# Kernel tuning notes

Measured on AMD Instinct MI355X. Metric: run time of the kernel, lower is better.

## Reference

```python
import jax, jax.numpy as jnp
import numpy as np
from jax import lax

NOISE_STD = 0.0005
ALPHA = 0.1
B, S, I, H, O = 128, 2000, 8, 512, 2
NUM_EXC, NUM_INH = 384, 128


def setup_inputs() -> dict:
    key = jax.random.key(0)
    ks = jax.random.split(key, 6)
    return {
        "input": jax.random.normal(ks[0], (B, S, I), dtype=jnp.float32),
        "noise": jax.random.normal(ks[1], (B, S, H), dtype=jnp.float32),
        "wi": jax.random.normal(ks[2], (I, H), dtype=jnp.float32) / np.sqrt(I),
        # excitatory rows in [0, 0.5], inhibitory rows in [-0.5, 0] (Dale's law)
        "wrec_exc": jax.random.uniform(ks[3], (NUM_EXC, H), dtype=jnp.float32, minval=0.0, maxval=0.5),
        "wrec_inh": jax.random.uniform(ks[4], (NUM_INH, H), dtype=jnp.float32, minval=-0.5, maxval=0.0),
        "wout": jax.random.normal(ks[5], (H, O), dtype=jnp.float32) / np.sqrt(H),
        "h0": jnp.zeros((H,), dtype=jnp.float32),
    }


def reference(input, noise, wi, wrec_exc, wrec_inh, wout, h0):
    batch = input.shape[0]
    # wrec rows: [exc sources; inh sources]
    wrec = jnp.concatenate([wrec_exc, wrec_inh], axis=0)  # [H, H]
    r0 = jnp.tanh(h0)  # [H]
    out0 = jnp.broadcast_to(r0 @ wout, (batch, wout.shape[1]))  # output[:, 0]
    h_init = jnp.broadcast_to(h0, (batch, h0.shape[0]))  # [B, H]
    # precompute input projection for steps 0..S-2 (last step's input unused)
    xproj = jnp.einsum("bsi,ih->sbh", input[:, :-1], wi)  # [S-1, B, H]
    noise_t = jnp.transpose(noise[:, :-1], (1, 0, 2))  # [S-1, B, H]

    def step(h, inp):
        x_t, n_t = inp
        r = jnp.tanh(h)
        h_new = h + NOISE_STD * n_t + ALPHA * (-h + r @ wrec.T + x_t)
        return h_new, jnp.tanh(h_new) @ wout  # emit output[:, i+1]

    _, outs = lax.scan(step, h_init, (xproj, noise_t))  # outs: [S-1, B, O]
    output = jnp.concatenate([out0[None], outs], axis=0)  # [S, B, O]
    return jnp.transpose(output, (1, 0, 2))  # [B, S, O]
```

## Files before the change

### kernel.cpp

```cpp
#include <hip/hip_runtime.h>
#include <cmath>


constexpr int kS = 2000, kI = 8, kH = 512, kO = 2;
constexpr float kNoiseStd = 0.0005f, kAlpha = 0.1f;

constexpr int GROUPS = 8;
constexpr int NSPL   = 2;
constexpr int JS     = 256;
constexpr int NTHR   = 512;
constexpr int NBLK   = GROUPS * NSPL;
constexpr int RSLOT  = 8192;

typedef _Float16 half8  __attribute__((ext_vector_type(8)));
typedef float    floatx4 __attribute__((ext_vector_type(4)));
typedef unsigned uintx4  __attribute__((ext_vector_type(4)));

#define MFMA16(A, B, C) __builtin_amdgcn_mfma_f32_16x16x32_f16((A), (B), (C), 0, 0, 0)
#define PIN8(a) asm volatile("" : "+v"((a)[0]), "+v"((a)[1]), "+v"((a)[2]), "+v"((a)[3]), \
                                   "+v"((a)[4]), "+v"((a)[5]), "+v"((a)[6]), "+v"((a)[7]))

static __device__ __forceinline__ unsigned ld_flag(const unsigned* p) {
  return __hip_atomic_load(p, __ATOMIC_RELAXED, __HIP_MEMORY_SCOPE_AGENT);
}
static __device__ __forceinline__ void st_flag(unsigned* p, unsigned v) {
  __hip_atomic_store(p, v, __ATOMIC_RELAXED, __HIP_MEMORY_SCOPE_AGENT);
}

static __device__ __forceinline__ float fast_tanh(float x) {
  const float ax = __builtin_fabsf(x);
  const float e = __builtin_amdgcn_exp2f(2.8853900817779268f * ax);
  const float r = __builtin_amdgcn_rcpf(e + 1.0f);
  return __builtin_copysignf(__builtin_fmaf(-2.0f, r, 1.0f), x);
}

__global__ __launch_bounds__(NTHR, 1) void rnn_k(
    const float* __restrict__ inp,
    const float* __restrict__ noise,
    const float* __restrict__ wi,
    const float* __restrict__ wexc,
    const float* __restrict__ winh,
    const float* __restrict__ wout,
    const float* __restrict__ h0,
    float* __restrict__ out,
    _Float16* __restrict__ rbuf,
    unsigned* __restrict__ flags)
{
  const int bid = blockIdx.x;
  const int g = bid & 7;
  const int c = bid >> 3;
  const int tid = threadIdx.x;
  const int w = tid >> 6;
  const int lane = tid & 63;
  const int l15 = lane & 15;
  const int lhi = lane >> 4;

  const int j0 = c * JS + w * 32 + l15;
  const int j1 = j0 + 16;
  const int ktp = c * 8 + w;
  const int jsub0 = l15 >> 3, jsub1 = 2 + (l15 >> 3), vv = l15 & 7;

  __shared__ _Float16 ldsA[2][RSLOT];
  __shared__ half8 ws_wout[16][64];
  __shared__ float ldsIN[16][kI];

  half8 wfo0[8], wfo1[8], wfp0[8], wfp1[8];
  {
    const float* wr0 = (j0 < 384) ? (wexc + (size_t)j0 * kH) : (winh + (size_t)(j0 - 384) * kH);
    const float* wr1 = (j1 < 384) ? (wexc + (size_t)j1 * kH) : (winh + (size_t)(j1 - 384) * kH);
    const int ko = (c * 8) * 32 + lhi * 8;
    const int kp = ((c ^ 1) * 8) * 32 + lhi * 8;
#pragma unroll
    for (int t = 0; t < 8; ++t) {
      half8 a, b, d, e;
#pragma unroll
      for (int v = 0; v < 8; ++v) {
        a[v] = (_Float16)wr0[ko + t * 32 + v];
        b[v] = (_Float16)wr1[ko + t * 32 + v];
        d[v] = (_Float16)wr0[kp + t * 32 + v];
        e[v] = (_Float16)wr1[kp + t * 32 + v];
      }
      wfo0[t] = a; wfo1[t] = b; wfp0[t] = d; wfp1[t] = e;
    }
    PIN8(wfo0); PIN8(wfo1); PIN8(wfp0); PIN8(wfp1);
  }

  float wiv0[8], wiv1[8];
#pragma unroll
  for (int i = 0; i < 8; ++i) { wiv0[i] = wi[i * kH + j0]; wiv1[i] = wi[i * kH + j1]; }

  if (c == 0 && w < 4) {
#pragma unroll
    for (int t = 0; t < 4; ++t) {
      const int kt = w * 4 + t;
      const int k0 = kt * 32 + lhi * 8;
      half8 hv;
#pragma unroll
      for (int v = 0; v < 8; ++v)
        hv[v] = (l15 < kO) ? (_Float16)wout[(size_t)(k0 + v) * kO + l15] : (_Float16)0.f;
      ws_wout[kt][lane] = hv;
    }
  }

  float hq0[4], hq1[4];
  {
    const float h00 = h0[j0], h01 = h0[j1];
#pragma unroll
    for (int q = 0; q < 4; ++q) { hq0[q] = h00; hq1[q] = h01; }
    const _Float16 r00 = (_Float16)fast_tanh(h00);
    const _Float16 r01 = (_Float16)fast_tanh(h01);
#pragma unroll
    for (int q = 0; q < 4; ++q) {
      const int bb = lhi * 4 + q;
      ldsA[0][ktp * 512 + (bb + 16 * jsub0) * 8 + vv] = r00;
      ldsA[0][ktp * 512 + (bb + 16 * jsub1) * 8 + vv] = r01;
    }
    const uintx4 pub = *(const uintx4*)((const char*)&ldsA[0][0] + ktp * 1024 + lane * 16);
    char* dst = (char*)rbuf + (size_t)(0 * GROUPS + g) * (RSLOT * 2) + ktp * 1024 + lane * 16;
    asm volatile("global_store_dwordx4 %0, %1, off sc0 sc1" :: "v"(dst), "v"(pub) : "memory");
  }
  __syncthreads();
  if (tid == 0) st_flag(&flags[(0 * GROUPS + g) * NSPL + c], 1u);

  for (int s = 0; s < kS; ++s) {
    const int cur = s & 1;
    const bool lastS = (s == kS - 1);
    if (lastS && c != 0) break;

    float nz0[4], nz1[4];
    float inv = 0.f;
    if (!lastS) {
#pragma unroll
      for (int q = 0; q < 4; ++q) {
        const int b = g * 16 + lhi * 4 + q;
        nz0[q] = noise[((size_t)b * kS + s) * kH + j0];
        nz1[q] = noise[((size_t)b * kS + s) * kH + j1];
      }
      if (w == 2 || w == 3) {
        const int ii = tid - 128;
        inv = inp[((size_t)(g * 16 + (ii >> 3)) * kS + s) * kI + (ii & 7)];
      }
    }

    {
      const unsigned need = (unsigned)(s + 1);
      const unsigned* fp = &flags[(cur * GROUPS + g) * NSPL + (c ^ 1)];
      while (ld_flag(fp) < need) {}
      asm volatile("" ::: "memory");
    }

    uintx4 pv;
    {
      const char* src = (const char*)rbuf + (size_t)(cur * GROUPS + g) * (RSLOT * 2)
                        + (c ^ 1) * 8192 + tid * 16;
      asm volatile("global_load_dwordx4 %0, %1, off sc0 sc1" : "=&v"(pv) : "v"(src) : "memory");
    }

    floatx4 a00 = {0,0,0,0}, a01 = {0,0,0,0}, a10 = {0,0,0,0}, a11 = {0,0,0,0};
    const char* base = (const char*)&ldsA[cur][0];
    const char* baseO = base + c * 8192;
    const char* baseP = base + (c ^ 1) * 8192;
#pragma unroll
    for (int t = 0; t < 8; t += 2) {
      const half8 f0 = *(const half8*)(baseO + t * 1024 + lane * 16);
      const half8 f1 = *(const half8*)(baseO + (t + 1) * 1024 + lane * 16);
      a00 = MFMA16(f0, wfo0[t], a00);
      a10 = MFMA16(f0, wfo1[t], a10);
      a01 = MFMA16(f1, wfo0[t + 1], a01);
      a11 = MFMA16(f1, wfo1[t + 1], a11);
    }
    __builtin_amdgcn_sched_barrier(0);
    asm volatile("s_waitcnt vmcnt(0)" : "+v"(pv) :: "memory");
    *(uintx4*)((char*)&ldsA[cur][0] + (c ^ 1) * 8192 + tid * 16) = pv;
    if (!lastS && (w == 2 || w == 3)) {
      const int ii = tid - 128;
      ldsIN[ii >> 3][ii & 7] = inv;
    }
    __syncthreads();

#pragma unroll
    for (int t = 0; t < 8; t += 2) {
      const half8 f0 = *(const half8*)(baseP + t * 1024 + lane * 16);
      const half8 f1 = *(const half8*)(baseP + (t + 1) * 1024 + lane * 16);
      a00 = MFMA16(f0, wfp0[t], a00);
      a10 = MFMA16(f0, wfp1[t], a10);
      a01 = MFMA16(f1, wfp0[t + 1], a01);
      a11 = MFMA16(f1, wfp1[t + 1], a11);
    }

    if (c == 0 && w == 7) {
      floatx4 oa = {0,0,0,0}, ob = {0,0,0,0};
#pragma unroll
      for (int kt = 0; kt < 16; kt += 2) {
        const half8 f0 = *(const half8*)(base + kt * 1024 + lane * 16);
        const half8 f1 = *(const half8*)(base + (kt + 1) * 1024 + lane * 16);
        oa = MFMA16(f0, ws_wout[kt][lane], oa);
        ob = MFMA16(f1, ws_wout[kt + 1][lane], ob);
      }
      if (l15 < kO) {
#pragma unroll
        for (int q = 0; q < 4; ++q)
          out[((size_t)(g * 16 + lhi * 4 + q) * kS + s) * kO + l15] = oa[q] + ob[q];
      }
    }

    if (!lastS) {
      _Float16* lA = &ldsA[cur ^ 1][0];
#pragma unroll
      for (int q = 0; q < 4; ++q) {
        const int bb = lhi * 4 + q;
        const floatx4 iv0 = *(const floatx4*)&ldsIN[bb][0];
        const floatx4 iv1 = *(const floatx4*)&ldsIN[bb][4];
        float x0 = 0.f, x1 = 0.f;
#pragma unroll
        for (int i = 0; i < 4; ++i) {
          x0 = fmaf(iv0[i], wiv0[i], x0); x0 = fmaf(iv1[i], wiv0[i + 4], x0);
          x1 = fmaf(iv0[i], wiv1[i], x1); x1 = fmaf(iv1[i], wiv1[i + 4], x1);
        }
        const float y0 = a00[q] + a01[q], y1 = a10[q] + a11[q];
        const float h0n = hq0[q] + kNoiseStd * nz0[q] + kAlpha * (-hq0[q] + y0 + x0);
        const float h1n = hq1[q] + kNoiseStd * nz1[q] + kAlpha * (-hq1[q] + y1 + x1);
        hq0[q] = h0n; hq1[q] = h1n;
        lA[ktp * 512 + (bb + 16 * jsub0) * 8 + vv] = (_Float16)fast_tanh(h0n);
        lA[ktp * 512 + (bb + 16 * jsub1) * 8 + vv] = (_Float16)fast_tanh(h1n);
      }
      const uintx4 pub = *(const uintx4*)((const char*)lA + ktp * 1024 + lane * 16);
      char* dst = (char*)rbuf + (size_t)((cur ^ 1) * GROUPS + g) * (RSLOT * 2)
                  + ktp * 1024 + lane * 16;
      asm volatile("global_store_dwordx4 %0, %1, off sc0 sc1" :: "v"(dst), "v"(pub) : "memory");
    }
    __syncthreads();
    if (!lastS && tid == 0)
      st_flag(&flags[((cur ^ 1) * GROUPS + g) * NSPL + c], (unsigned)(s + 2));
  }
}

extern "C" void kernel_launch(void* const* d_in, const int* in_sizes, int n_in,
                              void* d_out, int out_size, void* d_ws, size_t ws_size,
                              hipStream_t stream) {
  const float* inp   = (const float*)d_in[0];
  const float* noise = (const float*)d_in[1];
  const float* wi    = (const float*)d_in[2];
  const float* wexc  = (const float*)d_in[3];
  const float* winh  = (const float*)d_in[4];
  const float* wout  = (const float*)d_in[5];
  const float* h0    = (const float*)d_in[6];

  _Float16* rbuf = (_Float16*)d_ws;
  const size_t rbytes = (size_t)2 * GROUPS * RSLOT * sizeof(_Float16);
  unsigned* flags = (unsigned*)((char*)d_ws + rbytes);

  hipMemsetAsync(flags, 0, 2 * GROUPS * NSPL * sizeof(unsigned), stream);
  rnn_k<<<NBLK, NTHR, 0, stream>>>(inp, noise, wi, wexc, winh, wout, h0,
                                   (float*)d_out, rbuf, flags);
}
```

Before: 5.009 ms.

## Offload output projection to dedicated consumer blocks via ring buffer of states

Adds eight extra blocks, one per batch group, that compute the wout projection for each step. They read the published tanh states from a 4-slot ring buffer in global memory, using flags to know when a step is ready, and signal back once they have consumed a slot. This removes the output MFMA work and global stores from the critical path of the recurrent blocks. The cost is extra flag traffic, a possible stall when the ring fills up, and a larger workspace whose flags must be zeroed each launch.

```diff
diff --git a/kernel.cpp b/kernel.cpp
--- a/kernel.cpp
+++ b/kernel.cpp
@@ -9,8 +9,13 @@
 constexpr int NSPL   = 2;
 constexpr int JS     = 256;
 constexpr int NTHR   = 512;
-constexpr int NBLK   = GROUPS * NSPL;
-constexpr int RSLOT  = 8192;
+constexpr int NRNN   = GROUPS * NSPL;
+constexpr int NBLK   = NRNN + GROUPS;
+constexpr int RING   = 4;
+
+constexpr size_t OFF_FLG = (size_t)RING * GROUPS * 16384;
+constexpr size_t OFF_OPG = OFF_FLG + 128;
+constexpr size_t WS_END  = OFF_OPG + GROUPS * 128;
 
 typedef _Float16 half8  __attribute__((ext_vector_type(8)));
 typedef float    floatx4 __attribute__((ext_vector_type(4)));
@@ -43,13 +48,62 @@
     const float* __restrict__ wout,
     const float* __restrict__ h0,
     float* __restrict__ out,
-    _Float16* __restrict__ rbuf,
-    unsigned* __restrict__ flags)
+    char* __restrict__ ws)
 {
   const int bid = blockIdx.x;
+  const int tid = threadIdx.x;
+  unsigned* flg = (unsigned*)(ws + OFF_FLG);
+
+  if (bid >= NRNN) {
+    if (tid >= 64) return;
+    const int g = bid - NRNN;
+    const int lane = tid;
+    const int l15 = lane & 15;
+    const int lhi = lane >> 4;
+    unsigned* opg = (unsigned*)(ws + OFF_OPG) + g * 32;
+
+    half8 wf[16];
+#pragma unroll
+    for (int kt = 0; kt < 16; ++kt) {
+      const int k0 = kt * 32 + lhi * 8;
+      half8 hv;
+#pragma unroll
+      for (int v = 0; v < 8; ++v)
+        hv[v] = (l15 < kO) ? (_Float16)wout[(size_t)(k0 + v) * kO + l15] : (_Float16)0.f;
+      wf[kt] = hv;
+    }
+
+    for (int r = 0; r < kS; ++r) {
+      const unsigned need = (unsigned)(r + 1);
+      const unsigned* f0p = flg + ((r & 1) * GROUPS + g) * NSPL;
+      while (ld_flag(f0p) < need || ld_flag(f0p + 1) < need) {}
+      asm volatile("" ::: "memory");
+      const char* slot = ws + ((size_t)(r & (RING - 1)) * GROUPS + g) * 16384;
+      half8 rf[16];
+#pragma unroll
+      for (int kt = 0; kt < 16; ++kt)
+        asm volatile("global_load_dwordx4 %0, %1, off sc0 sc1"
+                     : "=&v"(rf[kt]) : "v"(slot + kt * 1024 + lane * 16) : "memory");
+      asm volatile("s_waitcnt vmcnt(0)" ::: "memory");
+      __builtin_amdgcn_sched_barrier(0);
+      st_flag(opg, (unsigned)(r + 1));
+      floatx4 oa = {0,0,0,0}, ob = {0,0,0,0};
+#pragma unroll
+      for (int kt = 0; kt < 16; kt += 2) {
+        oa = MFMA16(rf[kt],     wf[kt],     oa);
+        ob = MFMA16(rf[kt + 1], wf[kt + 1], ob);
+      }
+      if (l15 < kO) {
+#pragma unroll
+        for (int q = 0; q < 4; ++q)
+          out[((size_t)(g * 16 + lhi * 4 + q) * kS + r) * kO + l15] = oa[q] + ob[q];
+      }
+    }
+    return;
+  }
+
   const int g = bid & 7;
   const int c = bid >> 3;
-  const int tid = threadIdx.x;
   const int w = tid >> 6;
   const int lane = tid & 63;
   const int l15 = lane & 15;
@@ -59,9 +113,9 @@
   const int j1 = j0 + 16;
   const int ktp = c * 8 + w;
   const int jsub0 = l15 >> 3, jsub1 = 2 + (l15 >> 3), vv = l15 & 7;
-
-  __shared__ _Float16 ldsA[2][RSLOT];
-  __shared__ half8 ws_wout[16][64];
+  unsigned* opg = (unsigned*)(ws + OFF_OPG) + g * 32;
+
+  __shared__ _Float16 ldsA[2][8192];
   __shared__ float ldsIN[16][kI];
 
   half8 wfo0[8], wfo1[8], wfp0[8], wfp1[8];
@@ -89,19 +143,6 @@
 #pragma unroll
   for (int i = 0; i < 8; ++i) { wiv0[i] = wi[i * kH + j0]; wiv1[i] = wi[i * kH + j1]; }
 
-  if (c == 0 && w < 4) {
-#pragma unroll
-    for (int t = 0; t < 4; ++t) {
-      const int kt = w * 4 + t;
-      const int k0 = kt * 32 + lhi * 8;
-      half8 hv;
-#pragma unroll
-      for (int v = 0; v < 8; ++v)
-        hv[v] = (l15 < kO) ? (_Float16)wout[(size_t)(k0 + v) * kO + l15] : (_Float16)0.f;
-      ws_wout[kt][lane] = hv;
-    }
-  }
-
   float hq0[4], hq1[4];
   {
     const float h00 = h0[j0], h01 = h0[j1];
@@ -116,42 +157,40 @@
       ldsA[0][ktp * 512 + (bb + 16 * jsub1) * 8 + vv] = r01;
     }
     const uintx4 pub = *(const uintx4*)((const char*)&ldsA[0][0] + ktp * 1024 + lane * 16);
-    char* dst = (char*)rbuf + (size_t)(0 * GROUPS + g) * (RSLOT * 2) + ktp * 1024 + lane * 16;
+    char* dst = ws + (size_t)(0 * GROUPS + g) * 16384 + ktp * 1024 + lane * 16;
     asm volatile("global_store_dwordx4 %0, %1, off sc0 sc1" :: "v"(dst), "v"(pub) : "memory");
   }
   __syncthreads();
-  if (tid == 0) st_flag(&flags[(0 * GROUPS + g) * NSPL + c], 1u);
-
-  for (int s = 0; s < kS; ++s) {
+  if (tid == 0) st_flag(&flg[(0 * GROUPS + g) * NSPL + c], 1u);
+
+  for (int s = 0; s < kS - 1; ++s) {
     const int cur = s & 1;
-    const bool lastS = (s == kS - 1);
-    if (lastS && c != 0) break;
+
+    const unsigned opv = ld_flag(opg);
 
     float nz0[4], nz1[4];
     float inv = 0.f;
-    if (!lastS) {
-#pragma unroll
-      for (int q = 0; q < 4; ++q) {
-        const int b = g * 16 + lhi * 4 + q;
-        nz0[q] = noise[((size_t)b * kS + s) * kH + j0];
-        nz1[q] = noise[((size_t)b * kS + s) * kH + j1];
-      }
-      if (w == 2 || w == 3) {
-        const int ii = tid - 128;
-        inv = inp[((size_t)(g * 16 + (ii >> 3)) * kS + s) * kI + (ii & 7)];
-      }
+#pragma unroll
+    for (int q = 0; q < 4; ++q) {
+      const int b = g * 16 + lhi * 4 + q;
+      nz0[q] = noise[((size_t)b * kS + s) * kH + j0];
+      nz1[q] = noise[((size_t)b * kS + s) * kH + j1];
+    }
+    if (w == 2 || w == 3) {
+      const int ii = tid - 128;
+      inv = inp[((size_t)(g * 16 + (ii >> 3)) * kS + s) * kI + (ii & 7)];
     }
 
     {
       const unsigned need = (unsigned)(s + 1);
-      const unsigned* fp = &flags[(cur * GROUPS + g) * NSPL + (c ^ 1)];
+      const unsigned* fp = &flg[(cur * GROUPS + g) * NSPL + (c ^ 1)];
       while (ld_flag(fp) < need) {}
       asm volatile("" ::: "memory");
     }
 
     uintx4 pv;
     {
-      const char* src = (const char*)rbuf + (size_t)(cur * GROUPS + g) * (RSLOT * 2)
+      const char* src = ws + ((size_t)(s & (RING - 1)) * GROUPS + g) * 16384
                         + (c ^ 1) * 8192 + tid * 16;
       asm volatile("global_load_dwordx4 %0, %1, off sc0 sc1" : "=&v"(pv) : "v"(src) : "memory");
     }
@@ -172,7 +211,7 @@
     __builtin_amdgcn_sched_barrier(0);
     asm volatile("s_waitcnt vmcnt(0)" : "+v"(pv) :: "memory");
     *(uintx4*)((char*)&ldsA[cur][0] + (c ^ 1) * 8192 + tid * 16) = pv;
-    if (!lastS && (w == 2 || w == 3)) {
+    if (w == 2 || w == 3) {
       const int ii = tid - 128;
       ldsIN[ii >> 3][ii & 7] = inv;
     }
@@ -188,23 +227,7 @@
       a11 = MFMA16(f1, wfp1[t + 1], a11);
     }
 
-    if (c == 0 && w == 7) {
-      floatx4 oa = {0,0,0,0}, ob = {0,0,0,0};
-#pragma unroll
-      for (int kt = 0; kt < 16; kt += 2) {
-        const half8 f0 = *(const half8*)(base + kt * 1024 + lane * 16);
-        const half8 f1 = *(const half8*)(base + (kt + 1) * 1024 + lane * 16);
-        oa = MFMA16(f0, ws_wout[kt][lane], oa);
-        ob = MFMA16(f1, ws_wout[kt + 1][lane], ob);
-      }
-      if (l15 < kO) {
-#pragma unroll
-        for (int q = 0; q < 4; ++q)
-          out[((size_t)(g * 16 + lhi * 4 + q) * kS + s) * kO + l15] = oa[q] + ob[q];
-      }
-    }
-
-    if (!lastS) {
+    {
       _Float16* lA = &ldsA[cur ^ 1][0];
 #pragma unroll
       for (int q = 0; q < 4; ++q) {
@@ -224,14 +247,19 @@
         lA[ktp * 512 + (bb + 16 * jsub0) * 8 + vv] = (_Float16)fast_tanh(h0n);
         lA[ktp * 512 + (bb + 16 * jsub1) * 8 + vv] = (_Float16)fast_tanh(h1n);
       }
+      if (opv + (unsigned)RING < (unsigned)(s + 2)) {
+        const unsigned need = (unsigned)(s + 2 - RING);
+        while (ld_flag(opg) < need) {}
+        asm volatile("" ::: "memory");
+      }
       const uintx4 pub = *(const uintx4*)((const char*)lA + ktp * 1024 + lane * 16);
-      char* dst = (char*)rbuf + (size_t)((cur ^ 1) * GROUPS + g) * (RSLOT * 2)
+      char* dst = ws + ((size_t)((s + 1) & (RING - 1)) * GROUPS + g) * 16384
                   + ktp * 1024 + lane * 16;
       asm volatile("global_store_dwordx4 %0, %1, off sc0 sc1" :: "v"(dst), "v"(pub) : "memory");
     }
     __syncthreads();
-    if (!lastS && tid == 0)
-      st_flag(&flags[((cur ^ 1) * GROUPS + g) * NSPL + c], (unsigned)(s + 2));
+    if (tid == 0)
+      st_flag(&flg[((cur ^ 1) * GROUPS + g) * NSPL + c], (unsigned)(s + 2));
   }
 }
 
@@ -246,11 +274,7 @@
   const float* wout  = (const float*)d_in[5];
   const float* h0    = (const float*)d_in[6];
 
-  _Float16* rbuf = (_Float16*)d_ws;
-  const size_t rbytes = (size_t)2 * GROUPS * RSLOT * sizeof(_Float16);
-  unsigned* flags = (unsigned*)((char*)d_ws + rbytes);
-
-  hipMemsetAsync(flags, 0, 2 * GROUPS * NSPL * sizeof(unsigned), stream);
+  hipMemsetAsync((char*)d_ws + OFF_FLG, 0, WS_END - OFF_FLG, stream);
   rnn_k<<<NBLK, NTHR, 0, stream>>>(inp, noise, wi, wexc, winh, wout, h0,
-                                   (float*)d_out, rbuf, flags);
-}
+                                   (float*)d_out, (char*)d_ws);
+}
```

New measurement: 5.255 ms. +4.9%, slower.

## Merge split blocks into one 1024-thread block per group, stream weights from L2

Applied to the files above, without the earlier changes.

Replaces the two-block-per-batch-group split, which exchanged hidden states through global memory with flag spinning, with a single 1024-thread block per group that holds the full hidden state in LDS. This removes the cross-block handshake and global round trip each step. The recurrent weights no longer fit in registers, so they are converted to fp16 into a workspace once and re-streamed from global/L2 every step with double-buffered register chunks. Input projection weights move to LDS and the next step's input is prefetched. The cost is weight reload traffic on every step and only 8 blocks running.

```diff
diff --git a/kernel.cpp b/kernel.cpp
--- a/kernel.cpp
+++ b/kernel.cpp
@@ -6,26 +6,13 @@
 constexpr float kNoiseStd = 0.0005f, kAlpha = 0.1f;
 
 constexpr int GROUPS = 8;
-constexpr int NSPL   = 2;
-constexpr int JS     = 256;
-constexpr int NTHR   = 512;
-constexpr int NBLK   = GROUPS * NSPL;
-constexpr int RSLOT  = 8192;
+constexpr int NTHR   = 1024;
+constexpr int NBLK   = GROUPS;
 
 typedef _Float16 half8  __attribute__((ext_vector_type(8)));
 typedef float    floatx4 __attribute__((ext_vector_type(4)));
-typedef unsigned uintx4  __attribute__((ext_vector_type(4)));
 
 #define MFMA16(A, B, C) __builtin_amdgcn_mfma_f32_16x16x32_f16((A), (B), (C), 0, 0, 0)
-#define PIN8(a) asm volatile("" : "+v"((a)[0]), "+v"((a)[1]), "+v"((a)[2]), "+v"((a)[3]), \
-                                   "+v"((a)[4]), "+v"((a)[5]), "+v"((a)[6]), "+v"((a)[7]))
-
-static __device__ __forceinline__ unsigned ld_flag(const unsigned* p) {
-  return __hip_atomic_load(p, __ATOMIC_RELAXED, __HIP_MEMORY_SCOPE_AGENT);
-}
-static __device__ __forceinline__ void st_flag(unsigned* p, unsigned v) {
-  __hip_atomic_store(p, v, __ATOMIC_RELAXED, __HIP_MEMORY_SCOPE_AGENT);
-}
 
 static __device__ __forceinline__ float fast_tanh(float x) {
   const float ax = __builtin_fabsf(x);
@@ -34,7 +21,7 @@
   return __builtin_copysignf(__builtin_fmaf(-2.0f, r, 1.0f), x);
 }
 
-__global__ __launch_bounds__(NTHR, 1) void rnn_k(
+__global__ __launch_bounds__(NTHR, 4) void rnn_k(
     const float* __restrict__ inp,
     const float* __restrict__ noise,
     const float* __restrict__ wi,
@@ -43,53 +30,43 @@
     const float* __restrict__ wout,
     const float* __restrict__ h0,
     float* __restrict__ out,
-    _Float16* __restrict__ rbuf,
-    unsigned* __restrict__ flags)
+    _Float16* __restrict__ wf16)
 {
-  const int bid = blockIdx.x;
-  const int g = bid & 7;
-  const int c = bid >> 3;
+  const int g = blockIdx.x;
   const int tid = threadIdx.x;
   const int w = tid >> 6;
   const int lane = tid & 63;
   const int l15 = lane & 15;
   const int lhi = lane >> 4;
 
-  const int j0 = c * JS + w * 32 + l15;
+  const int j0 = w * 32 + l15;
   const int j1 = j0 + 16;
-  const int ktp = c * 8 + w;
   const int jsub0 = l15 >> 3, jsub1 = 2 + (l15 >> 3), vv = l15 & 7;
-
-  __shared__ _Float16 ldsA[2][RSLOT];
+  const int krot = (w >= 8) ? 8 : 0;
+
+  __shared__ _Float16 ldsA[2][8192];
   __shared__ half8 ws_wout[16][64];
-  __shared__ float ldsIN[16][kI];
-
-  half8 wfo0[8], wfo1[8], wfp0[8], wfp1[8];
+  __shared__ float ldsWI[512][8];
+  __shared__ float ldsIN[2][16][kI];
+
+  _Float16* wbase = wf16 + ((size_t)w * 64 + lane) * 16;
   {
     const float* wr0 = (j0 < 384) ? (wexc + (size_t)j0 * kH) : (winh + (size_t)(j0 - 384) * kH);
     const float* wr1 = (j1 < 384) ? (wexc + (size_t)j1 * kH) : (winh + (size_t)(j1 - 384) * kH);
-    const int ko = (c * 8) * 32 + lhi * 8;
-    const int kp = ((c ^ 1) * 8) * 32 + lhi * 8;
-#pragma unroll
-    for (int t = 0; t < 8; ++t) {
-      half8 a, b, d, e;
+#pragma unroll
+    for (int kt = 0; kt < 16; ++kt) {
+      half8 b0, b1;
 #pragma unroll
       for (int v = 0; v < 8; ++v) {
-        a[v] = (_Float16)wr0[ko + t * 32 + v];
-        b[v] = (_Float16)wr1[ko + t * 32 + v];
-        d[v] = (_Float16)wr0[kp + t * 32 + v];
-        e[v] = (_Float16)wr1[kp + t * 32 + v];
-      }
-      wfo0[t] = a; wfo1[t] = b; wfp0[t] = d; wfp1[t] = e;
-    }
-    PIN8(wfo0); PIN8(wfo1); PIN8(wfp0); PIN8(wfp1);
-  }
-
-  float wiv0[8], wiv1[8];
-#pragma unroll
-  for (int i = 0; i < 8; ++i) { wiv0[i] = wi[i * kH + j0]; wiv1[i] = wi[i * kH + j1]; }
-
-  if (c == 0 && w < 4) {
+        b0[v] = (_Float16)wr0[kt * 32 + lhi * 8 + v];
+        b1[v] = (_Float16)wr1[kt * 32 + lhi * 8 + v];
+      }
+      *(half8*)(wbase + (size_t)kt * 16384)     = b0;
+      *(half8*)(wbase + (size_t)kt * 16384 + 8) = b1;
+    }
+  }
+
+  if (w < 4) {
 #pragma unroll
     for (int t = 0; t < 4; ++t) {
       const int kt = w * 4 + t;
@@ -101,6 +78,14 @@
       ws_wout[kt][lane] = hv;
     }
   }
+  if (tid < 512) {
+#pragma unroll
+    for (int i = 0; i < 8; ++i) ldsWI[tid][i] = wi[i * kH + tid];
+  }
+  if (w == 2 || w == 3) {
+    const int ii = tid - 128;
+    ldsIN[0][ii >> 3][ii & 7] = inp[((size_t)(g * 16 + (ii >> 3)) * kS + 0) * kI + (ii & 7)];
+  }
 
   float hq0[4], hq1[4];
   {
@@ -112,83 +97,39 @@
 #pragma unroll
     for (int q = 0; q < 4; ++q) {
       const int bb = lhi * 4 + q;
-      ldsA[0][ktp * 512 + (bb + 16 * jsub0) * 8 + vv] = r00;
-      ldsA[0][ktp * 512 + (bb + 16 * jsub1) * 8 + vv] = r01;
-    }
-    const uintx4 pub = *(const uintx4*)((const char*)&ldsA[0][0] + ktp * 1024 + lane * 16);
-    char* dst = (char*)rbuf + (size_t)(0 * GROUPS + g) * (RSLOT * 2) + ktp * 1024 + lane * 16;
-    asm volatile("global_store_dwordx4 %0, %1, off sc0 sc1" :: "v"(dst), "v"(pub) : "memory");
+      ldsA[0][w * 512 + (bb + 16 * jsub0) * 8 + vv] = r00;
+      ldsA[0][w * 512 + (bb + 16 * jsub1) * 8 + vv] = r01;
+    }
   }
   __syncthreads();
-  if (tid == 0) st_flag(&flags[(0 * GROUPS + g) * NSPL + c], 1u);
+
+  half8 wA0[4], wA1[4], wB0[4], wB1[4];
+#pragma unroll
+  for (int t = 0; t < 4; ++t) {
+    const _Float16* p = wbase + (size_t)((t + krot) & 15) * 16384;
+    wA0[t] = *(const half8*)p; wA1[t] = *(const half8*)(p + 8);
+  }
+
+#define LDCHUNK(B0, B1, KTBASE)                                              \
+  _Pragma("unroll")                                                          \
+  for (int t = 0; t < 4; ++t) {                                              \
+    const _Float16* p = wbase + (size_t)(((KTBASE) + t + krot) & 15) * 16384; \
+    B0[t] = *(const half8*)p; B1[t] = *(const half8*)(p + 8);                \
+  }
+#define CK(KT, B0, B1)                                                       \
+  {                                                                          \
+    const int kk = ((KT) + krot) & 15;                                       \
+    const half8 f = *(const half8*)(base + kk * 1024 + lane * 16);           \
+    if ((KT) & 1) { a01 = MFMA16(f, B0, a01); a11 = MFMA16(f, B1, a11); }    \
+    else          { a00 = MFMA16(f, B0, a00); a10 = MFMA16(f, B1, a10); }    \
+  }
 
   for (int s = 0; s < kS; ++s) {
     const int cur = s & 1;
     const bool lastS = (s == kS - 1);
-    if (lastS && c != 0) break;
-
-    float nz0[4], nz1[4];
-    float inv = 0.f;
-    if (!lastS) {
-#pragma unroll
-      for (int q = 0; q < 4; ++q) {
-        const int b = g * 16 + lhi * 4 + q;
-        nz0[q] = noise[((size_t)b * kS + s) * kH + j0];
-        nz1[q] = noise[((size_t)b * kS + s) * kH + j1];
-      }
-      if (w == 2 || w == 3) {
-        const int ii = tid - 128;
-        inv = inp[((size_t)(g * 16 + (ii >> 3)) * kS + s) * kI + (ii & 7)];
-      }
-    }
-
-    {
-      const unsigned need = (unsigned)(s + 1);
-      const unsigned* fp = &flags[(cur * GROUPS + g) * NSPL + (c ^ 1)];
-      while (ld_flag(fp) < need) {}
-      asm volatile("" ::: "memory");
-    }
-
-    uintx4 pv;
-    {
-      const char* src = (const char*)rbuf + (size_t)(cur * GROUPS + g) * (RSLOT * 2)
-                        + (c ^ 1) * 8192 + tid * 16;
-      asm volatile("global_load_dwordx4 %0, %1, off sc0 sc1" : "=&v"(pv) : "v"(src) : "memory");
-    }
-
-    floatx4 a00 = {0,0,0,0}, a01 = {0,0,0,0}, a10 = {0,0,0,0}, a11 = {0,0,0,0};
     const char* base = (const char*)&ldsA[cur][0];
-    const char* baseO = base + c * 8192;
-    const char* baseP = base + (c ^ 1) * 8192;
-#pragma unroll
-    for (int t = 0; t < 8; t += 2) {
-      const half8 f0 = *(const half8*)(baseO + t * 1024 + lane * 16);
-      const half8 f1 = *(const half8*)(baseO + (t + 1) * 1024 + lane * 16);
-      a00 = MFMA16(f0, wfo0[t], a00);
-      a10 = MFMA16(f0, wfo1[t], a10);
-      a01 = MFMA16(f1, wfo0[t + 1], a01);
-      a11 = MFMA16(f1, wfo1[t + 1], a11);
-    }
-    __builtin_amdgcn_sched_barrier(0);
-    asm volatile("s_waitcnt vmcnt(0)" : "+v"(pv) :: "memory");
-    *(uintx4*)((char*)&ldsA[cur][0] + (c ^ 1) * 8192 + tid * 16) = pv;
-    if (!lastS && (w == 2 || w == 3)) {
-      const int ii = tid - 128;
-      ldsIN[ii >> 3][ii & 7] = inv;
-    }
-    __syncthreads();
-
-#pragma unroll
-    for (int t = 0; t < 8; t += 2) {
-      const half8 f0 = *(const half8*)(baseP + t * 1024 + lane * 16);
-      const half8 f1 = *(const half8*)(baseP + (t + 1) * 1024 + lane * 16);
-      a00 = MFMA16(f0, wfp0[t], a00);
-      a10 = MFMA16(f0, wfp1[t], a10);
-      a01 = MFMA16(f1, wfp0[t + 1], a01);
-      a11 = MFMA16(f1, wfp1[t + 1], a11);
-    }
-
-    if (c == 0 && w == 7) {
+
+    if (w == 15) {
       floatx4 oa = {0,0,0,0}, ob = {0,0,0,0};
 #pragma unroll
       for (int kt = 0; kt < 16; kt += 2) {
@@ -203,35 +144,65 @@
           out[((size_t)(g * 16 + lhi * 4 + q) * kS + s) * kO + l15] = oa[q] + ob[q];
       }
     }
-
-    if (!lastS) {
+    if (lastS) break;
+
+    float nz0[4], nz1[4];
+#pragma unroll
+    for (int q = 0; q < 4; ++q) {
+      const int b = g * 16 + lhi * 4 + q;
+      nz0[q] = noise[((size_t)b * kS + s) * kH + j0];
+      nz1[q] = noise[((size_t)b * kS + s) * kH + j1];
+    }
+    float invN = 0.f;
+    if (s < kS - 2 && (w == 2 || w == 3)) {
+      const int ii = tid - 128;
+      invN = inp[((size_t)(g * 16 + (ii >> 3)) * kS + (s + 1)) * kI + (ii & 7)];
+    }
+
+    floatx4 a00 = {0,0,0,0}, a01 = {0,0,0,0}, a10 = {0,0,0,0}, a11 = {0,0,0,0};
+    LDCHUNK(wB0, wB1, 4)
+    CK(0, wA0[0], wA1[0]) CK(1, wA0[1], wA1[1])
+    CK(2, wA0[2], wA1[2]) CK(3, wA0[3], wA1[3])
+    LDCHUNK(wA0, wA1, 8)
+    CK(4, wB0[0], wB1[0]) CK(5, wB0[1], wB1[1])
+    CK(6, wB0[2], wB1[2]) CK(7, wB0[3], wB1[3])
+    LDCHUNK(wB0, wB1, 12)
+    CK(8, wA0[0], wA1[0]) CK(9, wA0[1], wA1[1])
+    CK(10, wA0[2], wA1[2]) CK(11, wA0[3], wA1[3])
+    LDCHUNK(wA0, wA1, 0)
+    CK(12, wB0[0], wB1[0]) CK(13, wB0[1], wB1[1])
+    CK(14, wB0[2], wB1[2]) CK(15, wB0[3], wB1[3])
+
+    if (s < kS - 2 && (w == 2 || w == 3)) {
+      const int ii = tid - 128;
+      ldsIN[(s + 1) & 1][ii >> 3][ii & 7] = invN;
+    }
+    {
       _Float16* lA = &ldsA[cur ^ 1][0];
+      const floatx4 wv0a = *(const floatx4*)&ldsWI[j0][0];
+      const floatx4 wv0b = *(const floatx4*)&ldsWI[j0][4];
+      const floatx4 wv1a = *(const floatx4*)&ldsWI[j1][0];
+      const floatx4 wv1b = *(const floatx4*)&ldsWI[j1][4];
 #pragma unroll
       for (int q = 0; q < 4; ++q) {
         const int bb = lhi * 4 + q;
-        const floatx4 iv0 = *(const floatx4*)&ldsIN[bb][0];
-        const floatx4 iv1 = *(const floatx4*)&ldsIN[bb][4];
+        const floatx4 iv0 = *(const floatx4*)&ldsIN[cur][bb][0];
+        const floatx4 iv1 = *(const floatx4*)&ldsIN[cur][bb][4];
         float x0 = 0.f, x1 = 0.f;
 #pragma unroll
         for (int i = 0; i < 4; ++i) {
-          x0 = fmaf(iv0[i], wiv0[i], x0); x0 = fmaf(iv1[i], wiv0[i + 4], x0);
-          x1 = fmaf(iv0[i], wiv1[i], x1); x1 = fmaf(iv1[i], wiv1[i + 4], x1);
+          x0 = fmaf(iv0[i], wv0a[i], x0); x0 = fmaf(iv1[i], wv0b[i], x0);
+          x1 = fmaf(iv0[i], wv1a[i], x1); x1 = fmaf(iv1[i], wv1b[i], x1);
         }
         const float y0 = a00[q] + a01[q], y1 = a10[q] + a11[q];
         const float h0n = hq0[q] + kNoiseStd * nz0[q] + kAlpha * (-hq0[q] + y0 + x0);
         const float h1n = hq1[q] + kNoiseStd * nz1[q] + kAlpha * (-hq1[q] + y1 + x1);
         hq0[q] = h0n; hq1[q] = h1n;
-        lA[ktp * 512 + (bb + 16 * jsub0) * 8 + vv] = (_Float16)fast_tanh(h0n);
-        lA[ktp * 512 + (bb + 16 * jsub1) * 8 + vv] = (_Float16)fast_tanh(h1n);
-      }
-      const uintx4 pub = *(const uintx4*)((const char*)lA + ktp * 1024 + lane * 16);
-      char* dst = (char*)rbuf + (size_t)((cur ^ 1) * GROUPS + g) * (RSLOT * 2)
-                  + ktp * 1024 + lane * 16;
-      asm volatile("global_store_dwordx4 %0, %1, off sc0 sc1" :: "v"(dst), "v"(pub) : "memory");
+        lA[w * 512 + (bb + 16 * jsub0) * 8 + vv] = (_Float16)fast_tanh(h0n);
+        lA[w * 512 + (bb + 16 * jsub1) * 8 + vv] = (_Float16)fast_tanh(h1n);
+      }
     }
     __syncthreads();
-    if (!lastS && tid == 0)
-      st_flag(&flags[((cur ^ 1) * GROUPS + g) * NSPL + c], (unsigned)(s + 2));
   }
 }
 
@@ -246,11 +217,6 @@
   const float* wout  = (const float*)d_in[5];
   const float* h0    = (const float*)d_in[6];
 
-  _Float16* rbuf = (_Float16*)d_ws;
-  const size_t rbytes = (size_t)2 * GROUPS * RSLOT * sizeof(_Float16);
-  unsigned* flags = (unsigned*)((char*)d_ws + rbytes);
-
-  hipMemsetAsync(flags, 0, 2 * GROUPS * NSPL * sizeof(unsigned), stream);
   rnn_k<<<NBLK, NTHR, 0, stream>>>(inp, noise, wi, wexc, winh, wout, h0,
-                                   (float*)d_out, rbuf, flags);
+                                   (float*)d_out, (_Float16*)d_ws);
 }
```

Result: slower. 19.39 ms (+287.1%).
